# Kernel tuning notes

Hardware: AMD Instinct MI355X
Metric: run time of the kernel (lower is better)

## Reference

```python
import jax, jax.numpy as jnp
import numpy as np

B, N_OBJ, N_REL = 32, 16, 64
C, H, W = 1024, 50, 50
POOL, SR = 7, 2          # roi_pool_size, sampling_ratio
SPATIAL_SCALE = 1.0      # boxes are pre-scaled to fmap coords by scale_bboxes
DIMS = [1024, 1024, 512] # lin_obj_dim
IMG = 800                # square frame -> the original's h/w swap bug is a no-op


def setup_inputs() -> dict:
    key = jax.random.key(0)
    ks = jax.random.split(key, 8)
    fmap = jax.random.normal(ks[0], (B, C, H, W), dtype=jnp.float32)
    # valid boxes in image coords: x1<x2, y1<y2, inside [0, IMG]
    xy1 = jax.random.uniform(ks[1], (B, N_OBJ, 2), minval=0.0, maxval=600.0)
    wh = jax.random.uniform(ks[2], (B, N_OBJ, 2), minval=50.0, maxval=200.0)
    bboxes = jnp.concatenate([xy1, xy1 + wh], axis=-1).astype(jnp.float32)
    num_obj = jnp.full((B,), N_OBJ, dtype=jnp.int32)
    num_rels = jnp.full((B,), N_REL, dtype=jnp.int32)
    obj_pairs = jax.random.randint(ks[3], (B, N_REL, 2), 0, N_OBJ, dtype=jnp.int32)
    s1 = 1.0 / np.sqrt(DIMS[0]).astype(np.float32)
    s2 = 1.0 / np.sqrt(DIMS[1]).astype(np.float32)
    W1 = jax.random.uniform(ks[4], (DIMS[0], DIMS[1]), minval=-s1, maxval=s1, dtype=jnp.float32)
    b1 = jax.random.uniform(ks[5], (DIMS[1],), minval=-s1, maxval=s1, dtype=jnp.float32)
    W2 = jax.random.uniform(ks[6], (DIMS[1], DIMS[2]), minval=-s2, maxval=s2, dtype=jnp.float32)
    b2 = jax.random.uniform(ks[7], (DIMS[2],), minval=-s2, maxval=s2, dtype=jnp.float32)
    return dict(frame_feature_map=fmap, bboxes=bboxes, num_obj=num_obj,
                obj_pairs=obj_pairs, num_rels=num_rels,
                frame_width=IMG, frame_height=IMG,
                W1=W1, b1=b1, W2=W2, b2=b2)


def _interp_axis(coord, size):
    # torchvision RoIAlign (aligned=False) bilinear precompute along one axis
    valid = ((coord >= -1.0) & (coord <= size)).astype(coord.dtype)
    c = jnp.maximum(coord, 0.0)
    low = jnp.floor(c).astype(jnp.int32)
    at_edge = low >= size - 1
    low = jnp.minimum(low, size - 1)
    high = jnp.minimum(low + 1, size - 1)
    l = jnp.where(at_edge, 0.0, c - low.astype(coord.dtype))
    return low, high, 1.0 - l, l, valid


def roi_align(fmap, boxes, batch_idx, pool, sr, scale):
    # fmap [B,C,H,W]; boxes [R,4] (x1,y1,x2,y2); returns [R,pool,pool,C]
    _, Cc, Hc, Wc = fmap.shape
    x1, y1, x2, y2 = (boxes[:, i] * scale for i in range(4))
    roi_w = jnp.maximum(x2 - x1, 1.0)
    roi_h = jnp.maximum(y2 - y1, 1.0)
    # sample offsets (separable): bin ph, subsample iy -> ph + (iy+0.5)/sr, in bin units
    grid = (jnp.arange(pool, dtype=fmap.dtype)[:, None]
            + (jnp.arange(sr, dtype=fmap.dtype)[None, :] + 0.5) / sr).reshape(-1)  # [pool*sr]
    ys = y1[:, None] + (roi_h / pool)[:, None] * grid[None, :]  # [R, Sy]
    xs = x1[:, None] + (roi_w / pool)[:, None] * grid[None, :]  # [R, Sx]
    yl, yh, wy0, wy1, vy = _interp_axis(ys, Hc)
    xl, xh, wx0, wx1, vx = _interp_axis(xs, Wc)
    b = batch_idx[:, None, None]

    def g(yi, xi):
        # advanced indices split by ':' -> result [R, Sy, Sx, C]
        return fmap[b, :, yi[:, :, None], xi[:, None, :]]

    val = (wy0[:, :, None, None] * (wx0[:, None, :, None] * g(yl, xl)
                                    + wx1[:, None, :, None] * g(yl, xh))
           + wy1[:, :, None, None] * (wx0[:, None, :, None] * g(yh, xl)
                                      + wx1[:, None, :, None] * g(yh, xh)))
    val = val * (vy[:, :, None, None] * vx[:, None, :, None])  # out-of-range points -> 0
    R = boxes.shape[0]
    # average the sr x sr samples per bin (count = sr*sr, as in torchvision)
    return val.reshape(R, pool, sr, pool, sr, Cc).mean(axis=(2, 4))


def reference(frame_feature_map, bboxes, num_obj, obj_pairs, num_rels,
              frame_width, frame_height, W1, b1, W2, b2):
    Bn, Nmax = bboxes.shape[:2]
    # scale_bboxes -- faithful to the original (note its im_height/im_width swap)
    im_height, im_width = frame_width, frame_height
    fh, fw = frame_feature_map.shape[-2:]
    hs = fh / (im_height * 1.0)
    ws = fw / (im_width * 1.0)
    scaled = bboxes * jnp.asarray([ws, hs, ws, hs], dtype=bboxes.dtype)
    boxes = scaled.reshape(-1, 4)                              # full counts: concat == flatten
    batch_idx = jnp.repeat(jnp.arange(Bn, dtype=jnp.int32), Nmax)
    roi = roi_align(frame_feature_map, boxes, batch_idx, POOL, SR, SPATIAL_SCALE)  # [R,7,7,C]
    # lin_obj_net: Linear+ReLU stack applied on the channel (last) dim
    h = jax.nn.relu(roi @ W1 + b1)
    h = jax.nn.relu(h @ W2 + b2)                               # [R,7,7,512]
    feat = h.mean(axis=(1, 2))                                 # AvgPool2d(7x7) -> flatten: [R,512]
    # pair_features: gather two object vectors per relation and average
    obj_off = jnp.concatenate([jnp.zeros((1,), jnp.int32),
                               jnp.cumsum(num_obj)[:-1].astype(jnp.int32)])
    idx = obj_off[:, None, None] + obj_pairs                   # [B, N_REL, 2]
    f0 = feat[idx[..., 0].reshape(-1)]
    f1 = feat[idx[..., 1].reshape(-1)]
    return 0.5 * (f0 + f1)                                     # [sum(num_rels), 512]
```

## Files before the change

kernel.cpp:

```cpp
#include <hip/hip_runtime.h>

#define DEV __device__ __forceinline__

typedef unsigned short u16;
typedef short bf16x8 __attribute__((ext_vector_type(8)));
typedef float f32x4 __attribute__((ext_vector_type(4)));

#define BB    32
#define NOBJ  16
#define NREL  64
#define CCH   1024
#define FHW   50
#define HW    2500
#define NROI  512
#define MROWS 25088
#define D1    1024
#define D2    512

DEV u16 f2bf(float f) {
  unsigned u = __float_as_uint(f);
  unsigned r = (u + 0x7FFFu + ((u >> 16) & 1u)) >> 16;
  return (u16)r;
}
DEV float bf2f(u16 h) { return __uint_as_float((unsigned)h << 16); }
DEV unsigned pk(float lo, float hi) { return (unsigned)f2bf(lo) | ((unsigned)f2bf(hi) << 16); }

using gvoid = __attribute__((address_space(1))) const void;
using svoid = __attribute__((address_space(3))) void;
DEV void gl_lds16(const void* g, void* s) {
  __builtin_amdgcn_global_load_lds((gvoid*)g, (svoid*)s, 16, 0, 0);
}

DEV void transpose_tile(const float* __restrict__ in, u16* __restrict__ out,
                        int R, int C, int c0, int r0, int t) {
  __shared__ float tile[64][65];
  {
    const int rr = t >> 4;
    const int cq = (t & 15) * 4;
#pragma unroll
    for (int it = 0; it < 4; ++it) {
      int rl = rr + it * 16;
      int r = r0 + rl;
      int c = c0 + cq;
      if (c + 3 < C) {
        float4 v = *reinterpret_cast<const float4*>(&in[(size_t)r * C + c]);
        tile[rl][cq + 0] = v.x; tile[rl][cq + 1] = v.y;
        tile[rl][cq + 2] = v.z; tile[rl][cq + 3] = v.w;
      } else {
#pragma unroll
        for (int j = 0; j < 4; ++j)
          tile[rl][cq + j] = (c + j < C) ? in[(size_t)r * C + c + j] : 0.f;
      }
    }
  }
  __syncthreads();
  {
    const int c = t >> 2;
    const int rch = (t & 3) * 8;
    if (c0 + c < C) {
#pragma unroll
      for (int half = 0; half < 2; ++half) {
        int rb = rch + half * 32;
        uint4 o;
        o.x = pk(tile[rb + 0][c], tile[rb + 1][c]);
        o.y = pk(tile[rb + 2][c], tile[rb + 3][c]);
        o.z = pk(tile[rb + 4][c], tile[rb + 5][c]);
        o.w = pk(tile[rb + 6][c], tile[rb + 7][c]);
        *reinterpret_cast<uint4*>(&out[(size_t)(c0 + c) * R + r0 + rb]) = o;
      }
    }
  }
}

__global__ __launch_bounds__(256) void k_transpose_all(
    const float* __restrict__ W1, u16* __restrict__ W1b,
    const float* __restrict__ W2, u16* __restrict__ W2b,
    const float* __restrict__ fmap, u16* __restrict__ fmT) {
  const int bid = blockIdx.x;
  const int t = threadIdx.x;
  if (bid < 256) {
    transpose_tile(W1, W1b, D1, D1, (bid & 15) * 64, (bid >> 4) * 64, t);
  } else if (bid < 384) {
    const int b2 = bid - 256;
    transpose_tile(W2, W2b, D1, D2, (b2 & 7) * 64, (b2 >> 3) * 64, t);
  } else {
    const int f = bid - 384;
    const int b = f / 640;
    const int rem = f - b * 640;
    const int cx = rem % 40, ry = rem / 40;
    transpose_tile(fmap + (size_t)b * CCH * HW, fmT + (size_t)b * CCH * HW,
                   CCH, HW, cx * 64, ry * 64, t);
  }
}

DEV void acc8v(uint4 v, float w, float* a) {
  a[0] = fmaf(w, bf2f((u16)(v.x & 0xffffu)), a[0]);
  a[1] = fmaf(w, bf2f((u16)(v.x >> 16)), a[1]);
  a[2] = fmaf(w, bf2f((u16)(v.y & 0xffffu)), a[2]);
  a[3] = fmaf(w, bf2f((u16)(v.y >> 16)), a[3]);
  a[4] = fmaf(w, bf2f((u16)(v.z & 0xffffu)), a[4]);
  a[5] = fmaf(w, bf2f((u16)(v.z >> 16)), a[5]);
  a[6] = fmaf(w, bf2f((u16)(v.w & 0xffffu)), a[6]);
  a[7] = fmaf(w, bf2f((u16)(v.w >> 16)), a[7]);
}

template <int YC, int XC>
DEV void bin_accum(const u16* bt, const int* yrow, const float* yw,
                   const int* xidx, const float* xw, float* a) {
  uint4 v[YC * XC];
#pragma unroll
  for (int jy = 0; jy < YC; ++jy)
#pragma unroll
    for (int jx = 0; jx < XC; ++jx)
      v[jy * XC + jx] =
          *reinterpret_cast<const uint4*>(bt + (size_t)(yrow[jy] + xidx[jx]) * CCH);
#pragma unroll
  for (int jy = 0; jy < YC; ++jy)
#pragma unroll
    for (int jx = 0; jx < XC; ++jx)
      acc8v(v[jy * XC + jx], yw[jy] * xw[jx], a);
}

__global__ __launch_bounds__(128) void k_roi_fast(
    const u16* __restrict__ fmT, const float* __restrict__ bboxes,
    const int* __restrict__ pfw, const int* __restrict__ pfh,
    u16* __restrict__ Aout) {
  const int r = blockIdx.x;
  const int py = blockIdx.y;
  const int b = r >> 4;
  const int t = threadIdx.x;
  const int c0 = t * 8;

  __shared__ int s_cnt[2][7];
  __shared__ int s_idx[2][7][4];
  __shared__ float s_wgt[2][7][4];

  int axis = -1, p = 0;
  if (t < 7) { axis = 0; p = t; }
  else if (t >= 64 && t < 71) { axis = 1; p = t - 64; }
  if (axis >= 0) {
    float fwf = (float)pfw[0], fhf = (float)pfh[0];
    float hs = (float)FHW / fwf;
    float wsc = (float)FHW / fhf;
    float v1 = bboxes[r * 4 + (axis == 0 ? 1 : 0)] * (axis == 0 ? hs : wsc);
    float v2 = bboxes[r * 4 + (axis == 0 ? 3 : 2)] * (axis == 0 ? hs : wsc);
    float ext = fmaxf(v2 - v1, 1.0f);
    int idx[4]; float wgt[4]; int cnt = 0;
#pragma unroll
    for (int j = 0; j < 2; ++j) {
      float g = (float)p + (j ? 0.75f : 0.25f);
      float coord = v1 + (ext / 7.0f) * g;
      float valid = (coord >= -1.0f && coord <= 50.0f) ? 1.0f : 0.0f;
      float cc = fmaxf(coord, 0.0f);
      int lo = (int)floorf(cc);
      bool edge = (lo >= FHW - 1);
      lo = min(lo, FHW - 1);
      int hi = min(lo + 1, FHW - 1);
      float l = edge ? 0.0f : (cc - (float)lo);
      float pr_i[2]; int pr_x[2];
      pr_x[0] = lo; pr_i[0] = valid * (1.0f - l);
      pr_x[1] = hi; pr_i[1] = valid * l;
#pragma unroll
      for (int e = 0; e < 2; ++e) {
        if (pr_i[e] != 0.0f) {
          bool found = false;
          for (int q = 0; q < cnt; ++q)
            if (idx[q] == pr_x[e]) { wgt[q] += pr_i[e]; found = true; }
          if (!found) { idx[cnt] = pr_x[e]; wgt[cnt] = pr_i[e]; ++cnt; }
        }
      }
    }
    s_cnt[axis][p] = cnt;
#pragma unroll
    for (int q = 0; q < 4; ++q) {
      s_idx[axis][p][q] = (q < cnt) ? idx[q] : 0;
      s_wgt[axis][p][q] = (q < cnt) ? wgt[q] : 0.0f;
    }
  }
  __syncthreads();

  const u16* bt = fmT + (size_t)b * HW * CCH + c0;

  const int ycnt = s_cnt[0][py];
  int yrow[3]; float yw[3];
#pragma unroll
  for (int q = 0; q < 3; ++q) {
    yrow[q] = s_idx[0][py][q] * FHW;
    yw[q] = s_wgt[0][py][q];
  }

  for (int px = 0; px < 7; ++px) {
    const int xcnt = s_cnt[1][px];
    int xidx[3]; float xw[3];
#pragma unroll
    for (int q = 0; q < 3; ++q) {
      xidx[q] = s_idx[1][px][q];
      xw[q] = s_wgt[1][px][q];
    }
    float a[8] = {};
    switch (ycnt * 4 + xcnt) {
      case 1 * 4 + 1: bin_accum<1, 1>(bt, yrow, yw, xidx, xw, a); break;
      case 1 * 4 + 2: bin_accum<1, 2>(bt, yrow, yw, xidx, xw, a); break;
      case 1 * 4 + 3: bin_accum<1, 3>(bt, yrow, yw, xidx, xw, a); break;
      case 2 * 4 + 1: bin_accum<2, 1>(bt, yrow, yw, xidx, xw, a); break;
      case 2 * 4 + 2: bin_accum<2, 2>(bt, yrow, yw, xidx, xw, a); break;
      case 2 * 4 + 3: bin_accum<2, 3>(bt, yrow, yw, xidx, xw, a); break;
      case 3 * 4 + 1: bin_accum<3, 1>(bt, yrow, yw, xidx, xw, a); break;
      case 3 * 4 + 2: bin_accum<3, 2>(bt, yrow, yw, xidx, xw, a); break;
      case 3 * 4 + 3: bin_accum<3, 3>(bt, yrow, yw, xidx, xw, a); break;
      default: break;
    }
    u16* dst = Aout + (size_t)(r * 49 + py * 7 + px) * CCH + c0;
    uint4 o;
    o.x = pk(a[0] * 0.25f, a[1] * 0.25f);
    o.y = pk(a[2] * 0.25f, a[3] * 0.25f);
    o.z = pk(a[4] * 0.25f, a[5] * 0.25f);
    o.w = pk(a[6] * 0.25f, a[7] * 0.25f);
    *reinterpret_cast<uint4*>(dst) = o;
  }
}

template <int K, int N, int OBF>
__global__ __launch_bounds__(256) void k_gemm(
    const u16* __restrict__ A, const u16* __restrict__ Bt,
    const float* __restrict__ bias, void* __restrict__ Out) {
  __shared__ alignas(16) u16 As[128 * 32];
  __shared__ alignas(16) u16 Bs[128 * 32];
  const int t = threadIdx.x;
  const int lane = t & 63, w = t >> 6;
  const int wr = w >> 1, wc = w & 1;
  const int NT = N / 128;
  const int bid = blockIdx.x;
  const int chunk = (int)(gridDim.x >> 3);
  const int swz = (bid & 7) * chunk + (bid >> 3);
  const size_t m0 = (size_t)(swz / NT) * 128;
  const int n0 = (swz % NT) * 128;
  f32x4 acc[4][4] = {};
  const int srow = t >> 2;
  const int skc = (t & 3) * 8;
  for (int ks = 0; ks < K / 32; ++ks) {
    const int k0 = ks * 32;
    if (ks) __syncthreads();
    gl_lds16(A + (m0 + srow) * K + k0 + skc, &As[(size_t)t * 8]);
    gl_lds16(A + (m0 + 64 + srow) * K + k0 + skc, &As[(size_t)(t + 256) * 8]);
    gl_lds16(Bt + (size_t)(n0 + srow) * K + k0 + skc, &Bs[(size_t)t * 8]);
    gl_lds16(Bt + (size_t)(n0 + 64 + srow) * K + k0 + skc, &Bs[(size_t)(t + 256) * 8]);
    __syncthreads();
    const int koff = (lane >> 4) * 8;
    bf16x8 av[4], bv[4];
#pragma unroll
    for (int m = 0; m < 4; ++m)
      av[m] = *reinterpret_cast<const bf16x8*>(&As[(wr * 64 + m * 16 + (lane & 15)) * 32 + koff]);
#pragma unroll
    for (int n = 0; n < 4; ++n)
      bv[n] = *reinterpret_cast<const bf16x8*>(&Bs[(wc * 64 + n * 16 + (lane & 15)) * 32 + koff]);
#pragma unroll
    for (int m = 0; m < 4; ++m)
#pragma unroll
      for (int n = 0; n < 4; ++n)
        asm("v_mfma_f32_16x16x32_bf16 %0, %1, %2, %0"
            : "+v"(acc[m][n]) : "v"(av[m]), "v"(bv[n]));
  }
  asm volatile("s_nop 7\n\ts_nop 7\n\ts_nop 7" ::);
#pragma unroll
  for (int n = 0; n < 4; ++n) {
    int col = n0 + wc * 64 + n * 16 + (lane & 15);
    float bb = bias[col];
#pragma unroll
    for (int m = 0; m < 4; ++m) {
      size_t row0 = m0 + wr * 64 + m * 16 + (lane >> 4) * 4;
#pragma unroll
      for (int qq = 0; qq < 4; ++qq) {
        float v = fmaxf(acc[m][n][qq] + bb, 0.0f);
        if (OBF) ((u16*)Out)[(row0 + qq) * N + col] = f2bf(v);
        else     ((float*)Out)[(row0 + qq) * N + col] = v;
      }
    }
  }
}

__global__ __launch_bounds__(256) void k_mean(const u16* __restrict__ H2,
                                              float* __restrict__ feat) {
  const int r = blockIdx.x;
  const int c = threadIdx.x * 2;
  float s0 = 0.f, s1 = 0.f;
#pragma unroll
  for (int qq = 0; qq < 49; ++qq) {
    unsigned v = *reinterpret_cast<const unsigned*>(&H2[((size_t)r * 49 + qq) * D2 + c]);
    s0 += bf2f((u16)(v & 0xffffu));
    s1 += bf2f((u16)(v >> 16));
  }
  feat[(size_t)r * D2 + c] = s0 * (1.0f / 49.0f);
  feat[(size_t)r * D2 + c + 1] = s1 * (1.0f / 49.0f);
}

__global__ __launch_bounds__(256) void k_pairs(
    const float* __restrict__ feat, const int* __restrict__ num_obj,
    const int* __restrict__ pairs, float* __restrict__ out) {
  int r = blockIdx.x;
  int b = r >> 6;
  int off = 0;
  for (int i = 0; i < b; ++i) off += num_obj[i];
  int g0 = off + pairs[r * 2 + 0];
  int g1 = off + pairs[r * 2 + 1];
  for (int c = threadIdx.x; c < D2; c += 256) {
    out[(size_t)r * D2 + c] = 0.5f * (feat[(size_t)g0 * D2 + c] + feat[(size_t)g1 * D2 + c]);
  }
}

extern "C" void kernel_launch(void* const* d_in, const int* in_sizes, int n_in,
                              void* d_out, int out_size, void* d_ws, size_t ws_size,
                              hipStream_t stream) {
  const float* fmap = (const float*)d_in[0];
  const float* bboxes = (const float*)d_in[1];
  const int* num_obj = (const int*)d_in[2];
  const int* obj_pairs = (const int*)d_in[3];
  const int* pfw = (const int*)d_in[5];
  const int* pfh = (const int*)d_in[6];
  const float* W1 = (const float*)d_in[7];
  const float* b1 = (const float*)d_in[8];
  const float* W2 = (const float*)d_in[9];
  const float* b2 = (const float*)d_in[10];
  float* out = (float*)d_out;

  const size_t SZ_FMT = (size_t)BB * HW * CCH * 2;
  const size_t SZ_A   = (size_t)MROWS * D1 * 2;
  const size_t SZ_H1  = (size_t)MROWS * D1 * 2;
  const size_t SZ_W1B = (size_t)D1 * D1 * 2;
  const size_t SZ_W2B = (size_t)D1 * D2 * 2;

  char* ws = (char*)d_ws;
  u16* fmT = (u16*)ws;
  u16* A   = (u16*)(ws + SZ_FMT);
  u16* H1  = (u16*)(ws + SZ_FMT + SZ_A);
  u16* W1b = (u16*)(ws + SZ_FMT + SZ_A + SZ_H1);
  u16* W2b = (u16*)(ws + SZ_FMT + SZ_A + SZ_H1 + SZ_W1B);
  float* feat = (float*)(ws + SZ_FMT + SZ_A + SZ_H1 + SZ_W1B + SZ_W2B);
  u16* H2b = fmT;

  k_transpose_all<<<384 + BB * 640, 256, 0, stream>>>(W1, W1b, W2, W2b, fmap, fmT);

  k_roi_fast<<<dim3(NROI, 7), 128, 0, stream>>>(fmT, bboxes, pfw, pfh, A);

  k_gemm<D1, D1, 1><<<(MROWS / 128) * (D1 / 128), 256, 0, stream>>>(A, W1b, b1, (void*)H1);
  k_gemm<D1, D2, 1><<<(MROWS / 128) * (D2 / 128), 256, 0, stream>>>(H1, W2b, b2, (void*)H2b);
  k_mean<<<NROI, 256, 0, stream>>>(H2b, feat);
  k_pairs<<<BB * NREL, 256, 0, stream>>>(feat, num_obj, obj_pairs, out);
}
```

Measured before the change: 257.7 us.

## Widen GEMM K-tile to 64 with XOR-swizzled LDS layout

The MFMA GEMM now stages a K-depth of 64 per iteration instead of 32, halving the number of barrier/load rounds. It also XOR-swizzles the 16-byte chunks within each LDS row so the per-lane fragment reads avoid bank conflicts. Doubling LDS per block (32 KB total) may reduce occupancy, and there is still no double buffering, so loads and MFMAs remain serialized within each iteration.

```diff
diff --git a/kernel.cpp b/kernel.cpp
--- a/kernel.cpp
+++ b/kernel.cpp
@@ -224,8 +224,8 @@
 __global__ __launch_bounds__(256) void k_gemm(
     const u16* __restrict__ A, const u16* __restrict__ Bt,
     const float* __restrict__ bias, void* __restrict__ Out) {
-  __shared__ alignas(16) u16 As[128 * 32];
-  __shared__ alignas(16) u16 Bs[128 * 32];
+  __shared__ alignas(16) u16 As[128 * 64];
+  __shared__ alignas(16) u16 Bs[128 * 64];
   const int t = threadIdx.x;
   const int lane = t & 63, w = t >> 6;
   const int wr = w >> 1, wc = w & 1;
@@ -236,30 +236,50 @@
   const size_t m0 = (size_t)(swz / NT) * 128;
   const int n0 = (swz % NT) * 128;
   f32x4 acc[4][4] = {};
-  const int srow = t >> 2;
-  const int skc = (t & 3) * 8;
-  for (int ks = 0; ks < K / 32; ++ks) {
-    const int k0 = ks * 32;
-    if (ks) __syncthreads();
-    gl_lds16(A + (m0 + srow) * K + k0 + skc, &As[(size_t)t * 8]);
-    gl_lds16(A + (m0 + 64 + srow) * K + k0 + skc, &As[(size_t)(t + 256) * 8]);
-    gl_lds16(Bt + (size_t)(n0 + srow) * K + k0 + skc, &Bs[(size_t)t * 8]);
-    gl_lds16(Bt + (size_t)(n0 + 64 + srow) * K + k0 + skc, &Bs[(size_t)(t + 256) * 8]);
+
+  int srow[4], scol[4];
+#pragma unroll
+  for (int j = 0; j < 4; ++j) {
+    const int i = t + 256 * j;
+    srow[j] = i >> 3;
+    scol[j] = ((i & 7) ^ (srow[j] & 7)) * 8;
+  }
+
+  for (int kt = 0; kt < K / 64; ++kt) {
+    const int k0 = kt * 64;
+    if (kt) __syncthreads();
+#pragma unroll
+    for (int j = 0; j < 4; ++j) {
+      gl_lds16(A + (m0 + srow[j]) * K + k0 + scol[j], &As[(size_t)(t + 256 * j) * 8]);
+      gl_lds16(Bt + (size_t)(n0 + srow[j]) * K + k0 + scol[j], &Bs[(size_t)(t + 256 * j) * 8]);
+    }
     __syncthreads();
-    const int koff = (lane >> 4) * 8;
-    bf16x8 av[4], bv[4];
-#pragma unroll
-    for (int m = 0; m < 4; ++m)
-      av[m] = *reinterpret_cast<const bf16x8*>(&As[(wr * 64 + m * 16 + (lane & 15)) * 32 + koff]);
-#pragma unroll
-    for (int n = 0; n < 4; ++n)
-      bv[n] = *reinterpret_cast<const bf16x8*>(&Bs[(wc * 64 + n * 16 + (lane & 15)) * 32 + koff]);
-#pragma unroll
-    for (int m = 0; m < 4; ++m)
-#pragma unroll
-      for (int n = 0; n < 4; ++n)
-        asm("v_mfma_f32_16x16x32_bf16 %0, %1, %2, %0"
-            : "+v"(acc[m][n]) : "v"(av[m]), "v"(bv[n]));
+
+    bf16x8 av[2][4], bv[2][4];
+#pragma unroll
+    for (int ks = 0; ks < 2; ++ks) {
+      const int lchunk = ks * 4 + (lane >> 4);
+#pragma unroll
+      for (int m = 0; m < 4; ++m) {
+        const int row = wr * 64 + m * 16 + (lane & 15);
+        av[ks][m] = *reinterpret_cast<const bf16x8*>(
+            &As[row * 64 + (lchunk ^ (row & 7)) * 8]);
+      }
+#pragma unroll
+      for (int n = 0; n < 4; ++n) {
+        const int row = wc * 64 + n * 16 + (lane & 15);
+        bv[ks][n] = *reinterpret_cast<const bf16x8*>(
+            &Bs[row * 64 + (lchunk ^ (row & 7)) * 8]);
+      }
+    }
+#pragma unroll
+    for (int ks = 0; ks < 2; ++ks)
+#pragma unroll
+      for (int m = 0; m < 4; ++m)
+#pragma unroll
+        for (int n = 0; n < 4; ++n)
+          asm("v_mfma_f32_16x16x32_bf16 %0, %1, %2, %0"
+              : "+v"(acc[m][n]) : "v"(av[ks][m]), "v"(bv[ks][n]));
   }
   asm volatile("s_nop 7\n\ts_nop 7\n\ts_nop 7" ::);
 #pragma unroll
```

Result: faster. 252.1 us (-2.2%).
